# Kernel optimization log

Hardware: AMD Instinct MI355X
Metric: run time of the kernel (lower is better)

## Reference

```python
import jax, jax.numpy as jnp
import numpy as np

S, N_PER, N_FEAT, HID = 4, 12500, 1024, 256
N_STRUCT = 500


def setup_inputs() -> dict:
    key = jax.random.key(0)
    ks = jax.random.split(key, 11)
    sc = 1.0 / np.sqrt(N_FEAT)
    sh = 1.0 / np.sqrt(HID)
    return {
        "features": jax.random.normal(ks[0], (S, N_PER, N_FEAT), jnp.float32),
        "W1": jax.random.normal(ks[1], (S, N_FEAT, HID), jnp.float32) * sc,
        "b1": jax.random.normal(ks[2], (S, HID), jnp.float32) * 0.01,
        "W2": jax.random.normal(ks[3], (S, HID, HID), jnp.float32) * sh,
        "b2": jax.random.normal(ks[4], (S, HID), jnp.float32) * 0.01,
        "W3": jax.random.normal(ks[5], (S, HID, HID), jnp.float32) * sh,
        "b3": jax.random.normal(ks[6], (S, HID), jnp.float32) * 0.01,
        "W4": jax.random.normal(ks[7], (S, HID, 1), jnp.float32) * sh,
        "b4": jax.random.normal(ks[8], (S, 1), jnp.float32) * 0.01,
        "structure_idx": jax.random.randint(ks[9], (S, N_PER), 0, N_STRUCT, jnp.int64 if jax.config.jax_enable_x64 else jnp.int32).astype(jnp.int32),
        "n_structures": N_STRUCT,
    }


def reference(features, W1, b1, W2, b2, W3, b3, W4, b4, structure_idx, n_structures):
    # Per-species 4-layer SiLU MLP applied to species-grouped feature blocks.
    h = jax.nn.silu(jnp.einsum("snf,sfh->snh", features, W1) + b1[:, None, :])
    h = jax.nn.silu(jnp.einsum("snh,shk->snk", h, W2) + b2[:, None, :])
    h = jax.nn.silu(jnp.einsum("snh,shk->snk", h, W3) + b3[:, None, :])
    e = jnp.einsum("snh,sho->sno", h, W4) + b4[:, None, :]  # [S, N_per, 1]
    atomic_energies = e[..., 0].reshape(-1)                  # concat over species
    # index_add_ into per-structure energies
    energies = jax.ops.segment_sum(atomic_energies, structure_idx.reshape(-1), num_segments=n_structures)
    return energies
```

## Files before the change

kernel.cpp:

```cpp
#include <hip/hip_runtime.h>

typedef _Float16 f16;
typedef __attribute__((ext_vector_type(8))) _Float16 f16x8;
typedef __attribute__((ext_vector_type(4))) float f32x4;
typedef unsigned int u32;

#define S_      4
#define NPER    12500
#define NF      1024
#define HID     256
#define NSTRUCT 500
#define TM      64

#define GLB __attribute__((address_space(1)))
#define AS3 __attribute__((address_space(3)))

#define WAIT_VM(N)  asm volatile("s_waitcnt vmcnt(" #N ")" ::: "memory")
#define WAIT_LGKM() asm volatile("s_waitcnt lgkmcnt(0)" ::: "memory")
#define SCHED0()    __builtin_amdgcn_sched_barrier(0)
#define BARRIER()   do { __builtin_amdgcn_s_barrier(); SCHED0(); } while (0)

__global__ __launch_bounds__(256) void transpose_all_kernel(
    const float* __restrict__ W1, const float* __restrict__ W2,
    const float* __restrict__ W3,
    f16* __restrict__ w1t, f16* __restrict__ w2t, f16* __restrict__ w3t)
{
  const int z = blockIdx.z;
  const int layer = z >> 2, sp = z & 3;
  const float* in; f16* out; int K;
  if (layer == 0)      { in = W1; out = w1t; K = NF;  }
  else if (layer == 1) { in = W2; out = w2t; K = HID; }
  else                 { in = W3; out = w3t; K = HID; }
  if (blockIdx.x * 64 >= K) return;

  __shared__ float tile[64][65];
  const float* inp = in + (size_t)sp * K * HID;
  f16* outp = out + (size_t)sp * K * HID;
  const int k0 = blockIdx.x * 64;
  const int n0 = blockIdx.y * 64;
  const int t = threadIdx.x;
  {
    const int lk = t >> 2;
    const int nq = (t & 3) * 16;
    const float* src = inp + (size_t)(k0 + lk) * HID + n0 + nq;
    #pragma unroll
    for (int i = 0; i < 4; ++i) {
      float4 v = *(const float4*)(src + i * 4);
      tile[lk][nq + i * 4 + 0] = v.x;
      tile[lk][nq + i * 4 + 1] = v.y;
      tile[lk][nq + i * 4 + 2] = v.z;
      tile[lk][nq + i * 4 + 3] = v.w;
    }
  }
  __syncthreads();
  {
    const int ln = t >> 2;
    const int kq = (t & 3) * 16;
    f16* dst = outp + (size_t)(n0 + ln) * K + k0 + kq;
    f16x8 a, b;
    #pragma unroll
    for (int j = 0; j < 8; ++j) a[j] = (f16)tile[kq + j][ln];
    #pragma unroll
    for (int j = 0; j < 8; ++j) b[j] = (f16)tile[kq + 8 + j][ln];
    *(f16x8*)dst = a;
    *(f16x8*)(dst + 8) = b;
  }
}


__device__ __forceinline__ void zero_acc(f32x4 (&acc)[4][4]) {
  #pragma unroll
  for (int a = 0; a < 4; ++a)
    #pragma unroll
    for (int b = 0; b < 4; ++b)
      #pragma unroll
      for (int j = 0; j < 4; ++j) acc[a][b][j] = 0.f;
}

__device__ __forceinline__ void stage_w64(char* bS, const char* wbase, int c,
                                          int w, int lane)
{
  #pragma unroll
  for (int i = 0; i < 8; ++i) {
    const int seg  = w * 8 + i;
    const int rloc = lane >> 3;
    const int p    = lane & 7;
    const int row  = seg * 8 + rloc;
    const int slog = p ^ rloc;
    const char* gp = wbase + (size_t)row * (NF * 2) + (size_t)c * 128 + slog * 16;
    char* lp = bS + seg * 1024;
    __builtin_amdgcn_global_load_lds((const GLB u32*)gp, (AS3 u32*)lp, 16, 0, 0);
  }
}

__device__ __forceinline__ void stage_w32(char* wS, const char* wbase, int c,
                                          int w, int lane)
{
  #pragma unroll
  for (int i = 0; i < 4; ++i) {
    const int seg = w * 4 + i;
    const int row = seg * 16 + (lane >> 2);
    const int kbp = lane & 3;
    const int kb  = kbp ^ ((row >> 1) & 3);
    const char* gp = wbase + (size_t)row * (HID * 2) + c * 64 + kb * 16;
    char* lp = wS + seg * 1024;
    __builtin_amdgcn_global_load_lds((const GLB u32*)gp, (AS3 u32*)lp, 16, 0, 0);
  }
}

__device__ __forceinline__ void load_pa(float4 (&pa)[4], const float* fsrcT, int c)
{
  #pragma unroll
  for (int j = 0; j < 4; ++j)
    pa[j] = *(const float4*)(fsrcT + c * 64 + j * 4);
}

__device__ __forceinline__ void stage_feat64(char* aS, const float4 (&pa)[4], int t)
{
  const int r = t >> 2;
  #pragma unroll
  for (int wr = 0; wr < 2; ++wr) {
    f16x8 hv;
    const float4 lo = pa[wr * 2 + 0], hi = pa[wr * 2 + 1];
    hv[0]=(f16)lo.x; hv[1]=(f16)lo.y; hv[2]=(f16)lo.z; hv[3]=(f16)lo.w;
    hv[4]=(f16)hi.x; hv[5]=(f16)hi.y; hv[6]=(f16)hi.z; hv[7]=(f16)hi.w;
    const int slog = (t & 3) * 2 + wr;
    const int p = slog ^ (r & 7);
    *(f16x8*)(aS + r * 128 + p * 16) = hv;
  }
}

__device__ __forceinline__ void mfma64_a(f32x4 (&acc)[4][4], const char* aS,
                                         const char* bS, int w, int g, int l15)
{
  #pragma unroll
  for (int ks = 0; ks < 2; ++ks) {
    f16x8 af[4], bf[4];
    #pragma unroll
    for (int at = 0; at < 4; ++at) {
      const int rr = at * 16 + l15;
      const int p  = (ks * 4 + g) ^ (rr & 7);
      af[at] = *(const f16x8*)(aS + rr * 128 + p * 16);
    }
    #pragma unroll
    for (int bt = 0; bt < 4; ++bt) {
      const int nn = w * 64 + bt * 16 + l15;
      const int p  = (ks * 4 + g) ^ (nn & 7);
      bf[bt] = *(const f16x8*)(bS + nn * 128 + p * 16);
    }
    #pragma unroll
    for (int at = 0; at < 4; ++at)
      #pragma unroll
      for (int bt = 0; bt < 4; ++bt)
        acc[at][bt] = __builtin_amdgcn_mfma_f32_16x16x32_f16(af[at], bf[bt], acc[at][bt], 0, 0, 0);
  }
}

__device__ __forceinline__ void mfma32_h(f32x4 (&acc)[4][4], const char* hL, int c,
                                         const char* wS, int w, int g, int l15)
{
  f16x8 af[4], bf[4];
  #pragma unroll
  for (int at = 0; at < 4; ++at) {
    const int rr = at * 16 + l15;
    af[at] = *(const f16x8*)(hL + ((rr * 512 + c * 64 + g * 16) ^ ((rr & 7) << 4)));
  }
  #pragma unroll
  for (int bt = 0; bt < 4; ++bt) {
    const int nn = w * 64 + bt * 16 + l15;
    bf[bt] = *(const f16x8*)(wS + nn * 64 + ((g ^ ((nn >> 1) & 3)) * 16));
  }
  #pragma unroll
  for (int at = 0; at < 4; ++at)
    #pragma unroll
    for (int bt = 0; bt < 4; ++bt)
      acc[at][bt] = __builtin_amdgcn_mfma_f32_16x16x32_f16(af[at], bf[bt], acc[at][bt], 0, 0, 0);
}

__device__ __forceinline__ void silu_store(f32x4 (&acc)[4][4],
                                           const float* __restrict__ bias,
                                           char* hL, int w, int lane)
{
  const int g = lane >> 4, l15 = lane & 15;
  #pragma unroll
  for (int bt = 0; bt < 4; ++bt) {
    const int col = w * 64 + bt * 16 + l15;
    const float b = bias[col];
    #pragma unroll
    for (int at = 0; at < 4; ++at) {
      #pragma unroll
      for (int j = 0; j < 4; ++j) {
        const int row = at * 16 + g * 4 + j;
        float x = acc[at][bt][j] + b;
        x = x * __builtin_amdgcn_rcpf(1.f + __expf(-x));
        *(f16*)(hL + (((row * HID + col) * 2) ^ ((row & 7) << 4))) = (f16)x;
      }
    }
  }
}

#define L1_STEP(c, ASc, ASn, BSc, BSn, PAset, VMN, DOG, DOPA)   \
  do {                                                           \
    stage_feat64(ASn, PAset, t);                                 \
    if (DOG)  stage_w64(BSn, w1s, (c) + 1, w, lane);             \
    if (DOPA) load_pa(PAset, fsrcT, (c) + 4);                    \
    WAIT_VM(VMN); SCHED0();                                      \
    mfma64_a(acc, ASc, BSc, w, g, l15);                          \
    WAIT_LGKM(); BARRIER();                                      \
  } while (0)

#define HID_ST(c, WSc, WSstg, wsrc, cs)                          \
  do {                                                           \
    WAIT_VM(8); SCHED0();                                        \
    mfma32_h(acc, hL, c, WSc, w, g, l15);                        \
    WAIT_LGKM(); SCHED0();                                       \
    stage_w32(WSstg, wsrc, cs, w, lane);                         \
  } while (0)

__global__ __launch_bounds__(256, 2) void mlp_fused_kernel(
    const float* __restrict__ feats,
    const float* __restrict__ b1g,
    const float* __restrict__ b2g,
    const float* __restrict__ b3g,
    const float* __restrict__ w4g,
    const float* __restrict__ b4g,
    const int*   __restrict__ sidxg,
    const f16*   __restrict__ w1t,
    const f16*   __restrict__ w2t,
    const f16*   __restrict__ w3t,
    float*       __restrict__ outg)
{
  __shared__ char arena[80 * 1024];
  char* aS0 = arena;
  char* aS1 = arena + 8 * 1024;
  char* bS0 = arena + 16 * 1024;
  char* bS1 = arena + 48 * 1024;
  char* hL  = arena;
  char* wS0 = arena + 32 * 1024;
  char* wS1 = arena + 48 * 1024;
  char* wS2 = arena + 64 * 1024;

  const int s    = blockIdx.y;
  const int row0 = blockIdx.x * TM;
  const int t    = threadIdx.x;
  const int lane = t & 63;
  const int w    = t >> 6;
  const int g    = lane >> 4;
  const int l15  = lane & 15;

  const int gr   = row0 + (t >> 2);
  const bool valid = gr < NPER;
  const int grc  = valid ? gr : (NPER - 1);
  const float* fsrcT = feats + ((size_t)s * NPER + grc) * NF + (t & 3) * 16;
  const char*  w1s   = (const char*)(w1t + (size_t)s * HID * NF);
  const char*  w2s   = (const char*)(w2t + (size_t)s * HID * HID);
  const char*  w3s   = (const char*)(w3t + (size_t)s * HID * HID);

  f32x4 acc[4][4];
  zero_acc(acc);

  float4 pf[4], paA[4], paB[4], paC[4];
  load_pa(pf, fsrcT, 0);
  stage_w64(bS0, w1s, 0, w, lane);
  load_pa(paA, fsrcT, 1);
  load_pa(paB, fsrcT, 2);
  load_pa(paC, fsrcT, 3);
  stage_feat64(aS0, pf, t);
  WAIT_LGKM(); BARRIER();

  L1_STEP(0,  aS0, aS1, bS0, bS1, paA, 20, 1, 1);
  L1_STEP(1,  aS1, aS0, bS1, bS0, paB, 16, 1, 1);
  L1_STEP(2,  aS0, aS1, bS0, bS1, paC, 16, 1, 1);
  L1_STEP(3,  aS1, aS0, bS1, bS0, paA, 16, 1, 1);
  L1_STEP(4,  aS0, aS1, bS0, bS1, paB, 16, 1, 1);
  L1_STEP(5,  aS1, aS0, bS1, bS0, paC, 16, 1, 1);
  L1_STEP(6,  aS0, aS1, bS0, bS1, paA, 16, 1, 1);
  L1_STEP(7,  aS1, aS0, bS1, bS0, paB, 16, 1, 1);
  L1_STEP(8,  aS0, aS1, bS0, bS1, paC, 16, 1, 1);
  L1_STEP(9,  aS1, aS0, bS1, bS0, paA, 16, 1, 1);
  L1_STEP(10, aS0, aS1, bS0, bS1, paB, 16, 1, 1);
  L1_STEP(11, aS1, aS0, bS1, bS0, paC, 16, 1, 1);
  L1_STEP(12, aS0, aS1, bS0, bS1, paA, 12, 1, 0);
  L1_STEP(13, aS1, aS0, bS1, bS0, paB,  8, 1, 0);
  L1_STEP(14, aS0, aS1, bS0, bS1, paC,  8, 1, 0);
  {
    stage_w32(wS0, w2s, 0, w, lane);
    WAIT_VM(4); SCHED0();
    mfma64_a(acc, aS1, bS1, w, g, l15);
    WAIT_LGKM(); BARRIER();
  }

  silu_store(acc, b1g + s * HID, hL, w, lane);
  zero_acc(acc);
  stage_w32(wS1, w2s, 1, w, lane);
  stage_w32(wS2, w2s, 2, w, lane);
  WAIT_LGKM(); BARRIER();

  HID_ST(0, wS0, wS0, w2s, 3);
  HID_ST(1, wS1, wS1, w2s, 4);
  HID_ST(2, wS2, wS2, w2s, 5);
  HID_ST(3, wS0, wS0, w2s, 6);
  HID_ST(4, wS1, wS1, w2s, 7);
  HID_ST(5, wS2, wS2, w3s, 0);
  HID_ST(6, wS0, wS0, w3s, 1);
  HID_ST(7, wS1, wS1, w3s, 2);
  BARRIER();
  silu_store(acc, b2g + s * HID, hL, w, lane);
  zero_acc(acc);
  WAIT_LGKM(); BARRIER();

  HID_ST(0, wS2, wS2, w3s, 3);
  HID_ST(1, wS0, wS0, w3s, 4);
  HID_ST(2, wS1, wS1, w3s, 5);
  HID_ST(3, wS2, wS2, w3s, 6);
  HID_ST(4, wS0, wS0, w3s, 7);
  { WAIT_VM(8); SCHED0(); mfma32_h(acc, hL, 5, wS1, w, g, l15); }
  { WAIT_VM(4); SCHED0(); mfma32_h(acc, hL, 6, wS2, w, g, l15); }
  { WAIT_VM(0); SCHED0(); mfma32_h(acc, hL, 7, wS0, w, g, l15); }
  BARRIER();
  silu_store(acc, b3g + s * HID, hL, w, lane);
  WAIT_LGKM(); BARRIER();

  {
    const int row = t >> 2;
    const int q   = t & 3;
    const float* w4 = w4g + s * HID;
    float sum = 0.f;
    #pragma unroll
    for (int j8 = 0; j8 < 64; j8 += 8) {
      const int k = q * 64 + j8;
      f16x8 hv = *(const f16x8*)(hL + (((row * HID + k) * 2) ^ ((row & 7) << 4)));
      float4 wa = *(const float4*)(w4 + k);
      float4 wb = *(const float4*)(w4 + k + 4);
      sum += (float)hv[0] * wa.x + (float)hv[1] * wa.y + (float)hv[2] * wa.z + (float)hv[3] * wa.w
           + (float)hv[4] * wb.x + (float)hv[5] * wb.y + (float)hv[6] * wb.z + (float)hv[7] * wb.w;
    }
    sum += __shfl_xor(sum, 1);
    sum += __shfl_xor(sum, 2);
    if (q == 0 && valid) {
      atomicAdd(&outg[sidxg[s * NPER + gr]], sum + b4g[s]);
    }
  }
}

extern "C" void kernel_launch(void* const* d_in, const int* in_sizes, int n_in,
                              void* d_out, int out_size, void* d_ws, size_t ws_size,
                              hipStream_t stream)
{
  const float* feats = (const float*)d_in[0];
  const float* W1    = (const float*)d_in[1];
  const float* b1    = (const float*)d_in[2];
  const float* W2    = (const float*)d_in[3];
  const float* b2    = (const float*)d_in[4];
  const float* W3    = (const float*)d_in[5];
  const float* b3    = (const float*)d_in[6];
  const float* W4    = (const float*)d_in[7];
  const float* b4    = (const float*)d_in[8];
  const int*   sidx  = (const int*)d_in[9];
  float* out = (float*)d_out;

  f16* w1t = (f16*)d_ws;
  f16* w2t = w1t + (size_t)S_ * HID * NF;
  f16* w3t = w2t + (size_t)S_ * HID * HID;

  hipMemsetAsync(d_out, 0, NSTRUCT * sizeof(float), stream);
  transpose_all_kernel<<<dim3(16, 4, 12), 256, 0, stream>>>(W1, W2, W3, w1t, w2t, w3t);
  mlp_fused_kernel<<<dim3((NPER + TM - 1) / TM, S_), 256, 0, stream>>>(
      feats, b1, b2, b3, W4, b4, sidx, w1t, w2t, w3t, out);
}
```

Baseline: 108.3 us.

## Single-buffer weight LDS stages to cut shared memory and allow three blocks per CU

Replaces the double-buffered W1 tile and triple-buffered W2/W3 tiles with single LDS buffers, shrinking shared memory from 80KB to 48KB and raising launch bounds to 3 blocks per CU. Each step now runs the MFMA on the current buffer, then overwrites that buffer with the next weight chunk. The intent is more resident blocks to hide latency. The cost is that weight loads no longer overlap the MFMA work inside a block, and the vmcnt waits are tightened to match.

After: 192.7 us. +77.9%, slower.

```diff
diff --git a/kernel.cpp b/kernel.cpp
--- a/kernel.cpp
+++ b/kernel.cpp
@@ -199,25 +199,26 @@
   }
 }
 
-#define L1_STEP(c, ASc, ASn, BSc, BSn, PAset, VMN, DOG, DOPA)   \
+#define L1_STEP(c, ASc, ASn, PAset, VMN, DOG, DOPA)              \
   do {                                                           \
+    WAIT_VM(VMN); SCHED0();                                      \
+    mfma64_a(acc, ASc, bS, w, g, l15);                           \
+    WAIT_LGKM(); SCHED0();                                       \
+    if (DOG)  stage_w64(bS, w1s, (c) + 1, w, lane);              \
     stage_feat64(ASn, PAset, t);                                 \
-    if (DOG)  stage_w64(BSn, w1s, (c) + 1, w, lane);             \
     if (DOPA) load_pa(PAset, fsrcT, (c) + 4);                    \
-    WAIT_VM(VMN); SCHED0();                                      \
-    mfma64_a(acc, ASc, BSc, w, g, l15);                          \
     WAIT_LGKM(); BARRIER();                                      \
   } while (0)
 
-#define HID_ST(c, WSc, WSstg, wsrc, cs)                          \
+#define HID_ST(c, wsrc, cs, DOG)                                 \
   do {                                                           \
-    WAIT_VM(8); SCHED0();                                        \
-    mfma32_h(acc, hL, c, WSc, w, g, l15);                        \
+    WAIT_VM(0); SCHED0();                                        \
+    mfma32_h(acc, hL, c, wS, w, g, l15);                         \
     WAIT_LGKM(); SCHED0();                                       \
-    stage_w32(WSstg, wsrc, cs, w, lane);                         \
+    if (DOG) stage_w32(wS, wsrc, cs, w, lane);                   \
   } while (0)
 
-__global__ __launch_bounds__(256, 2) void mlp_fused_kernel(
+__global__ __launch_bounds__(256, 3) void mlp_fused_kernel(
     const float* __restrict__ feats,
     const float* __restrict__ b1g,
     const float* __restrict__ b2g,
@@ -230,15 +231,12 @@
     const f16*   __restrict__ w3t,
     float*       __restrict__ outg)
 {
-  __shared__ char arena[80 * 1024];
+  __shared__ char arena[48 * 1024];
   char* aS0 = arena;
   char* aS1 = arena + 8 * 1024;
-  char* bS0 = arena + 16 * 1024;
-  char* bS1 = arena + 48 * 1024;
+  char* bS  = arena + 16 * 1024;
   char* hL  = arena;
-  char* wS0 = arena + 32 * 1024;
-  char* wS1 = arena + 48 * 1024;
-  char* wS2 = arena + 64 * 1024;
+  char* wS  = arena + 32 * 1024;
 
   const int s    = blockIdx.y;
   const int row0 = blockIdx.x * TM;
@@ -261,62 +259,60 @@
 
   float4 pf[4], paA[4], paB[4], paC[4];
   load_pa(pf, fsrcT, 0);
-  stage_w64(bS0, w1s, 0, w, lane);
+  stage_w64(bS, w1s, 0, w, lane);
   load_pa(paA, fsrcT, 1);
   load_pa(paB, fsrcT, 2);
   load_pa(paC, fsrcT, 3);
   stage_feat64(aS0, pf, t);
   WAIT_LGKM(); BARRIER();
 
-  L1_STEP(0,  aS0, aS1, bS0, bS1, paA, 20, 1, 1);
-  L1_STEP(1,  aS1, aS0, bS1, bS0, paB, 16, 1, 1);
-  L1_STEP(2,  aS0, aS1, bS0, bS1, paC, 16, 1, 1);
-  L1_STEP(3,  aS1, aS0, bS1, bS0, paA, 16, 1, 1);
-  L1_STEP(4,  aS0, aS1, bS0, bS1, paB, 16, 1, 1);
-  L1_STEP(5,  aS1, aS0, bS1, bS0, paC, 16, 1, 1);
-  L1_STEP(6,  aS0, aS1, bS0, bS1, paA, 16, 1, 1);
-  L1_STEP(7,  aS1, aS0, bS1, bS0, paB, 16, 1, 1);
-  L1_STEP(8,  aS0, aS1, bS0, bS1, paC, 16, 1, 1);
-  L1_STEP(9,  aS1, aS0, bS1, bS0, paA, 16, 1, 1);
-  L1_STEP(10, aS0, aS1, bS0, bS1, paB, 16, 1, 1);
-  L1_STEP(11, aS1, aS0, bS1, bS0, paC, 16, 1, 1);
-  L1_STEP(12, aS0, aS1, bS0, bS1, paA, 12, 1, 0);
-  L1_STEP(13, aS1, aS0, bS1, bS0, paB,  8, 1, 0);
-  L1_STEP(14, aS0, aS1, bS0, bS1, paC,  8, 1, 0);
+  L1_STEP(0,  aS0, aS1, paA, 12, 1, 1);
+  L1_STEP(1,  aS1, aS0, paB,  4, 1, 1);
+  L1_STEP(2,  aS0, aS1, paC,  4, 1, 1);
+  L1_STEP(3,  aS1, aS0, paA,  4, 1, 1);
+  L1_STEP(4,  aS0, aS1, paB,  4, 1, 1);
+  L1_STEP(5,  aS1, aS0, paC,  4, 1, 1);
+  L1_STEP(6,  aS0, aS1, paA,  4, 1, 1);
+  L1_STEP(7,  aS1, aS0, paB,  4, 1, 1);
+  L1_STEP(8,  aS0, aS1, paC,  4, 1, 1);
+  L1_STEP(9,  aS1, aS0, paA,  4, 1, 1);
+  L1_STEP(10, aS0, aS1, paB,  4, 1, 1);
+  L1_STEP(11, aS1, aS0, paC,  4, 1, 1);
+  L1_STEP(12, aS0, aS1, paA,  4, 1, 0);
+  L1_STEP(13, aS1, aS0, paB,  0, 1, 0);
+  L1_STEP(14, aS0, aS1, paC,  0, 1, 0);
   {
-    stage_w32(wS0, w2s, 0, w, lane);
-    WAIT_VM(4); SCHED0();
-    mfma64_a(acc, aS1, bS1, w, g, l15);
+    WAIT_VM(0); SCHED0();
+    mfma64_a(acc, aS1, bS, w, g, l15);
     WAIT_LGKM(); BARRIER();
   }
 
+  stage_w32(wS, w2s, 0, w, lane);
   silu_store(acc, b1g + s * HID, hL, w, lane);
   zero_acc(acc);
-  stage_w32(wS1, w2s, 1, w, lane);
-  stage_w32(wS2, w2s, 2, w, lane);
   WAIT_LGKM(); BARRIER();
 
-  HID_ST(0, wS0, wS0, w2s, 3);
-  HID_ST(1, wS1, wS1, w2s, 4);
-  HID_ST(2, wS2, wS2, w2s, 5);
-  HID_ST(3, wS0, wS0, w2s, 6);
-  HID_ST(4, wS1, wS1, w2s, 7);
-  HID_ST(5, wS2, wS2, w3s, 0);
-  HID_ST(6, wS0, wS0, w3s, 1);
-  HID_ST(7, wS1, wS1, w3s, 2);
+  HID_ST(0, w2s, 1, 1);
+  HID_ST(1, w2s, 2, 1);
+  HID_ST(2, w2s, 3, 1);
+  HID_ST(3, w2s, 4, 1);
+  HID_ST(4, w2s, 5, 1);
+  HID_ST(5, w2s, 6, 1);
+  HID_ST(6, w2s, 7, 1);
+  HID_ST(7, w3s, 0, 1);
   BARRIER();
   silu_store(acc, b2g + s * HID, hL, w, lane);
   zero_acc(acc);
   WAIT_LGKM(); BARRIER();
 
-  HID_ST(0, wS2, wS2, w3s, 3);
-  HID_ST(1, wS0, wS0, w3s, 4);
-  HID_ST(2, wS1, wS1, w3s, 5);
-  HID_ST(3, wS2, wS2, w3s, 6);
-  HID_ST(4, wS0, wS0, w3s, 7);
-  { WAIT_VM(8); SCHED0(); mfma32_h(acc, hL, 5, wS1, w, g, l15); }
-  { WAIT_VM(4); SCHED0(); mfma32_h(acc, hL, 6, wS2, w, g, l15); }
-  { WAIT_VM(0); SCHED0(); mfma32_h(acc, hL, 7, wS0, w, g, l15); }
+  HID_ST(0, w3s, 1, 1);
+  HID_ST(1, w3s, 2, 1);
+  HID_ST(2, w3s, 3, 1);
+  HID_ST(3, w3s, 4, 1);
+  HID_ST(4, w3s, 5, 1);
+  HID_ST(5, w3s, 6, 1);
+  HID_ST(6, w3s, 7, 1);
+  HID_ST(7, w3s, 0, 0);
   BARRIER();
   silu_store(acc, b3g + s * HID, hL, w, lane);
   WAIT_LGKM(); BARRIER();
```

## Double row tile to 128 with 512 threads; stream hidden-layer weights via registers

Applied to the files above, without the earlier changes.

The fused MLP kernel now processes 128 rows per block with 8 waves arranged as 2 row groups by 4 column groups. Each W1 tile staged in LDS is therefore reused across twice as many rows, and the layer-1 pipeline switches to a single A buffer with a reordered stage/compute phase. The W2/W3 LDS staging is removed: each wave loads its B fragments for the hidden layers directly from global memory into double-buffered registers. This cuts W1 traffic per row and LDS round-trips for the hidden layers, at the cost of more register pressure, fewer blocks in the grid, and exposed global-load latency in the hidden layers.

New measurement: 183.1 us. +69.0%, slower.

```diff
diff --git a/kernel.cpp b/kernel.cpp
--- a/kernel.cpp
+++ b/kernel.cpp
@@ -10,7 +10,7 @@
 #define NF      1024
 #define HID     256
 #define NSTRUCT 500
-#define TM      64
+#define TM      128
 
 #define GLB __attribute__((address_space(1)))
 #define AS3 __attribute__((address_space(3)))
@@ -81,29 +81,14 @@
                                           int w, int lane)
 {
   #pragma unroll
-  for (int i = 0; i < 8; ++i) {
-    const int seg  = w * 8 + i;
+  for (int i = 0; i < 4; ++i) {
+    const int seg  = w * 4 + i;
     const int rloc = lane >> 3;
     const int p    = lane & 7;
     const int row  = seg * 8 + rloc;
     const int slog = p ^ rloc;
     const char* gp = wbase + (size_t)row * (NF * 2) + (size_t)c * 128 + slog * 16;
     char* lp = bS + seg * 1024;
-    __builtin_amdgcn_global_load_lds((const GLB u32*)gp, (AS3 u32*)lp, 16, 0, 0);
-  }
-}
-
-__device__ __forceinline__ void stage_w32(char* wS, const char* wbase, int c,
-                                          int w, int lane)
-{
-  #pragma unroll
-  for (int i = 0; i < 4; ++i) {
-    const int seg = w * 4 + i;
-    const int row = seg * 16 + (lane >> 2);
-    const int kbp = lane & 3;
-    const int kb  = kbp ^ ((row >> 1) & 3);
-    const char* gp = wbase + (size_t)row * (HID * 2) + c * 64 + kb * 16;
-    char* lp = wS + seg * 1024;
     __builtin_amdgcn_global_load_lds((const GLB u32*)gp, (AS3 u32*)lp, 16, 0, 0);
   }
 }
@@ -131,20 +116,21 @@
 }
 
 __device__ __forceinline__ void mfma64_a(f32x4 (&acc)[4][4], const char* aS,
-                                         const char* bS, int w, int g, int l15)
+                                         const char* bS, int rgrp, int cg,
+                                         int g, int l15)
 {
   #pragma unroll
   for (int ks = 0; ks < 2; ++ks) {
     f16x8 af[4], bf[4];
     #pragma unroll
     for (int at = 0; at < 4; ++at) {
-      const int rr = at * 16 + l15;
+      const int rr = rgrp * 64 + at * 16 + l15;
       const int p  = (ks * 4 + g) ^ (rr & 7);
       af[at] = *(const f16x8*)(aS + rr * 128 + p * 16);
     }
     #pragma unroll
     for (int bt = 0; bt < 4; ++bt) {
-      const int nn = w * 64 + bt * 16 + l15;
+      const int nn = cg * 64 + bt * 16 + l15;
       const int p  = (ks * 4 + g) ^ (nn & 7);
       bf[bt] = *(const f16x8*)(bS + nn * 128 + p * 16);
     }
@@ -156,19 +142,25 @@
   }
 }
 
+__device__ __forceinline__ void load_bh(f16x8 (&bf)[4], const f16* wsrc, int c,
+                                        int cg, int g, int l15)
+{
+  #pragma unroll
+  for (int bt = 0; bt < 4; ++bt) {
+    const int nn = cg * 64 + bt * 16 + l15;
+    bf[bt] = *(const f16x8*)(wsrc + (size_t)nn * HID + c * 32 + g * 8);
+  }
+}
+
 __device__ __forceinline__ void mfma32_h(f32x4 (&acc)[4][4], const char* hL, int c,
-                                         const char* wS, int w, int g, int l15)
-{
-  f16x8 af[4], bf[4];
+                                         const f16x8 (&bf)[4], int rgrp,
+                                         int g, int l15)
+{
+  f16x8 af[4];
   #pragma unroll
   for (int at = 0; at < 4; ++at) {
-    const int rr = at * 16 + l15;
+    const int rr = rgrp * 64 + at * 16 + l15;
     af[at] = *(const f16x8*)(hL + ((rr * 512 + c * 64 + g * 16) ^ ((rr & 7) << 4)));
-  }
-  #pragma unroll
-  for (int bt = 0; bt < 4; ++bt) {
-    const int nn = w * 64 + bt * 16 + l15;
-    bf[bt] = *(const f16x8*)(wS + nn * 64 + ((g ^ ((nn >> 1) & 3)) * 16));
   }
   #pragma unroll
   for (int at = 0; at < 4; ++at)
@@ -179,18 +171,18 @@
 
 __device__ __forceinline__ void silu_store(f32x4 (&acc)[4][4],
                                            const float* __restrict__ bias,
-                                           char* hL, int w, int lane)
+                                           char* hL, int rgrp, int cg, int lane)
 {
   const int g = lane >> 4, l15 = lane & 15;
   #pragma unroll
   for (int bt = 0; bt < 4; ++bt) {
-    const int col = w * 64 + bt * 16 + l15;
+    const int col = cg * 64 + bt * 16 + l15;
     const float b = bias[col];
     #pragma unroll
     for (int at = 0; at < 4; ++at) {
       #pragma unroll
       for (int j = 0; j < 4; ++j) {
-        const int row = at * 16 + g * 4 + j;
+        const int row = rgrp * 64 + at * 16 + g * 4 + j;
         float x = acc[at][bt][j] + b;
         x = x * __builtin_amdgcn_rcpf(1.f + __expf(-x));
         *(f16*)(hL + (((row * HID + col) * 2) ^ ((row & 7) << 4))) = (f16)x;
@@ -199,25 +191,18 @@
   }
 }
 
-#define L1_STEP(c, ASc, ASn, BSc, BSn, PAset, VMN, DOG, DOPA)   \
+#define L1_PH(c, BSc, PAset, DOPA, DOG, VMN)                     \
   do {                                                           \
-    stage_feat64(ASn, PAset, t);                                 \
-    if (DOG)  stage_w64(BSn, w1s, (c) + 1, w, lane);             \
-    if (DOPA) load_pa(PAset, fsrcT, (c) + 4);                    \
+    mfma64_a(acc, aS, BSc, rgrp, cg, g, l15);                    \
+    WAIT_LGKM(); BARRIER();                                      \
+    stage_feat64(aS, PAset, t);                                  \
+    if (DOPA) load_pa(PAset, fsrcT, (c) + 3);                    \
+    if (DOG)  stage_w64(BSc, w1s, (c) + 2, w, lane);             \
     WAIT_VM(VMN); SCHED0();                                      \
-    mfma64_a(acc, ASc, BSc, w, g, l15);                          \
     WAIT_LGKM(); BARRIER();                                      \
   } while (0)
 
-#define HID_ST(c, WSc, WSstg, wsrc, cs)                          \
-  do {                                                           \
-    WAIT_VM(8); SCHED0();                                        \
-    mfma32_h(acc, hL, c, WSc, w, g, l15);                        \
-    WAIT_LGKM(); SCHED0();                                       \
-    stage_w32(WSstg, wsrc, cs, w, lane);                         \
-  } while (0)
-
-__global__ __launch_bounds__(256, 2) void mlp_fused_kernel(
+__global__ __launch_bounds__(512, 4) void mlp_fused_kernel(
     const float* __restrict__ feats,
     const float* __restrict__ b1g,
     const float* __restrict__ b2g,
@@ -231,20 +216,18 @@
     float*       __restrict__ outg)
 {
   __shared__ char arena[80 * 1024];
-  char* aS0 = arena;
-  char* aS1 = arena + 8 * 1024;
+  char* aS  = arena;
   char* bS0 = arena + 16 * 1024;
   char* bS1 = arena + 48 * 1024;
   char* hL  = arena;
-  char* wS0 = arena + 32 * 1024;
-  char* wS1 = arena + 48 * 1024;
-  char* wS2 = arena + 64 * 1024;
 
   const int s    = blockIdx.y;
   const int row0 = blockIdx.x * TM;
   const int t    = threadIdx.x;
   const int lane = t & 63;
   const int w    = t >> 6;
+  const int rgrp = w >> 2;
+  const int cg   = w & 3;
   const int g    = lane >> 4;
   const int l15  = lane & 15;
 
@@ -253,72 +236,72 @@
   const int grc  = valid ? gr : (NPER - 1);
   const float* fsrcT = feats + ((size_t)s * NPER + grc) * NF + (t & 3) * 16;
   const char*  w1s   = (const char*)(w1t + (size_t)s * HID * NF);
-  const char*  w2s   = (const char*)(w2t + (size_t)s * HID * HID);
-  const char*  w3s   = (const char*)(w3t + (size_t)s * HID * HID);
+  const f16*   w2s   = w2t + (size_t)s * HID * HID;
+  const f16*   w3s   = w3t + (size_t)s * HID * HID;
 
   f32x4 acc[4][4];
+  f16x8 bfA[4], bfB[4];
   zero_acc(acc);
 
-  float4 pf[4], paA[4], paB[4], paC[4];
-  load_pa(pf, fsrcT, 0);
-  stage_w64(bS0, w1s, 0, w, lane);
+  float4 pf[4], paA[4], paB[4];
+  load_pa(pf,  fsrcT, 0);
   load_pa(paA, fsrcT, 1);
   load_pa(paB, fsrcT, 2);
-  load_pa(paC, fsrcT, 3);
-  stage_feat64(aS0, pf, t);
+  stage_w64(bS0, w1s, 0, w, lane);
+  stage_w64(bS1, w1s, 1, w, lane);
+  stage_feat64(aS, pf, t);
+  WAIT_VM(4); SCHED0();
   WAIT_LGKM(); BARRIER();
 
-  L1_STEP(0,  aS0, aS1, bS0, bS1, paA, 20, 1, 1);
-  L1_STEP(1,  aS1, aS0, bS1, bS0, paB, 16, 1, 1);
-  L1_STEP(2,  aS0, aS1, bS0, bS1, paC, 16, 1, 1);
-  L1_STEP(3,  aS1, aS0, bS1, bS0, paA, 16, 1, 1);
-  L1_STEP(4,  aS0, aS1, bS0, bS1, paB, 16, 1, 1);
-  L1_STEP(5,  aS1, aS0, bS1, bS0, paC, 16, 1, 1);
-  L1_STEP(6,  aS0, aS1, bS0, bS1, paA, 16, 1, 1);
-  L1_STEP(7,  aS1, aS0, bS1, bS0, paB, 16, 1, 1);
-  L1_STEP(8,  aS0, aS1, bS0, bS1, paC, 16, 1, 1);
-  L1_STEP(9,  aS1, aS0, bS1, bS0, paA, 16, 1, 1);
-  L1_STEP(10, aS0, aS1, bS0, bS1, paB, 16, 1, 1);
-  L1_STEP(11, aS1, aS0, bS1, bS0, paC, 16, 1, 1);
-  L1_STEP(12, aS0, aS1, bS0, bS1, paA, 12, 1, 0);
-  L1_STEP(13, aS1, aS0, bS1, bS0, paB,  8, 1, 0);
-  L1_STEP(14, aS0, aS1, bS0, bS1, paC,  8, 1, 0);
+  L1_PH(0,  bS0, paA, 1, 1, 8);
+  L1_PH(1,  bS1, paB, 1, 1, 8);
+  L1_PH(2,  bS0, paA, 1, 1, 8);
+  L1_PH(3,  bS1, paB, 1, 1, 8);
+  L1_PH(4,  bS0, paA, 1, 1, 8);
+  L1_PH(5,  bS1, paB, 1, 1, 8);
+  L1_PH(6,  bS0, paA, 1, 1, 8);
+  L1_PH(7,  bS1, paB, 1, 1, 8);
+  L1_PH(8,  bS0, paA, 1, 1, 8);
+  L1_PH(9,  bS1, paB, 1, 1, 8);
+  L1_PH(10, bS0, paA, 1, 1, 8);
+  L1_PH(11, bS1, paB, 1, 1, 8);
+  L1_PH(12, bS0, paA, 1, 1, 8);
+  L1_PH(13, bS1, paB, 0, 1, 4);
+  L1_PH(14, bS0, paA, 0, 0, 0);
   {
-    stage_w32(wS0, w2s, 0, w, lane);
-    WAIT_VM(4); SCHED0();
-    mfma64_a(acc, aS1, bS1, w, g, l15);
+    mfma64_a(acc, aS, bS1, rgrp, cg, g, l15);
+    load_bh(bfA, w2s, 0, cg, g, l15);
+    load_bh(bfB, w2s, 1, cg, g, l15);
     WAIT_LGKM(); BARRIER();
   }
 
-  silu_store(acc, b1g + s * HID, hL, w, lane);
-  zero_acc(acc);
-  stage_w32(wS1, w2s, 1, w, lane);
-  stage_w32(wS2, w2s, 2, w, lane);
-  WAIT_LGKM(); BARRIER();
-
-  HID_ST(0, wS0, wS0, w2s, 3);
-  HID_ST(1, wS1, wS1, w2s, 4);
-  HID_ST(2, wS2, wS2, w2s, 5);
-  HID_ST(3, wS0, wS0, w2s, 6);
-  HID_ST(4, wS1, wS1, w2s, 7);
-  HID_ST(5, wS2, wS2, w3s, 0);
-  HID_ST(6, wS0, wS0, w3s, 1);
-  HID_ST(7, wS1, wS1, w3s, 2);
-  BARRIER();
-  silu_store(acc, b2g + s * HID, hL, w, lane);
+  silu_store(acc, b1g + s * HID, hL, rgrp, cg, lane);
   zero_acc(acc);
   WAIT_LGKM(); BARRIER();
 
-  HID_ST(0, wS2, wS2, w3s, 3);
-  HID_ST(1, wS0, wS0, w3s, 4);
-  HID_ST(2, wS1, wS1, w3s, 5);
-  HID_ST(3, wS2, wS2, w3s, 6);
-  HID_ST(4, wS0, wS0, w3s, 7);
-  { WAIT_VM(8); SCHED0(); mfma32_h(acc, hL, 5, wS1, w, g, l15); }
-  { WAIT_VM(4); SCHED0(); mfma32_h(acc, hL, 6, wS2, w, g, l15); }
-  { WAIT_VM(0); SCHED0(); mfma32_h(acc, hL, 7, wS0, w, g, l15); }
+  mfma32_h(acc, hL, 0, bfA, rgrp, g, l15);  load_bh(bfA, w2s, 2, cg, g, l15);
+  mfma32_h(acc, hL, 1, bfB, rgrp, g, l15);  load_bh(bfB, w2s, 3, cg, g, l15);
+  mfma32_h(acc, hL, 2, bfA, rgrp, g, l15);  load_bh(bfA, w2s, 4, cg, g, l15);
+  mfma32_h(acc, hL, 3, bfB, rgrp, g, l15);  load_bh(bfB, w2s, 5, cg, g, l15);
+  mfma32_h(acc, hL, 4, bfA, rgrp, g, l15);  load_bh(bfA, w2s, 6, cg, g, l15);
+  mfma32_h(acc, hL, 5, bfB, rgrp, g, l15);  load_bh(bfB, w2s, 7, cg, g, l15);
+  mfma32_h(acc, hL, 6, bfA, rgrp, g, l15);  load_bh(bfA, w3s, 0, cg, g, l15);
+  mfma32_h(acc, hL, 7, bfB, rgrp, g, l15);  load_bh(bfB, w3s, 1, cg, g, l15);
   BARRIER();
-  silu_store(acc, b3g + s * HID, hL, w, lane);
+  silu_store(acc, b2g + s * HID, hL, rgrp, cg, lane);
+  zero_acc(acc);
+  WAIT_LGKM(); BARRIER();
+
+  mfma32_h(acc, hL, 0, bfA, rgrp, g, l15);  load_bh(bfA, w3s, 2, cg, g, l15);
+  mfma32_h(acc, hL, 1, bfB, rgrp, g, l15);  load_bh(bfB, w3s, 3, cg, g, l15);
+  mfma32_h(acc, hL, 2, bfA, rgrp, g, l15);  load_bh(bfA, w3s, 4, cg, g, l15);
+  mfma32_h(acc, hL, 3, bfB, rgrp, g, l15);  load_bh(bfB, w3s, 5, cg, g, l15);
+  mfma32_h(acc, hL, 4, bfA, rgrp, g, l15);  load_bh(bfA, w3s, 6, cg, g, l15);
+  mfma32_h(acc, hL, 5, bfB, rgrp, g, l15);  load_bh(bfB, w3s, 7, cg, g, l15);
+  mfma32_h(acc, hL, 6, bfA, rgrp, g, l15);
+  mfma32_h(acc, hL, 7, bfB, rgrp, g, l15);
+  BARRIER();
+  silu_store(acc, b3g + s * HID, hL, rgrp, cg, lane);
   WAIT_LGKM(); BARRIER();
 
   {
@@ -365,6 +348,6 @@
 
   hipMemsetAsync(d_out, 0, NSTRUCT * sizeof(float), stream);
   transpose_all_kernel<<<dim3(16, 4, 12), 256, 0, stream>>>(W1, W2, W3, w1t, w2t, w3t);
-  mlp_fused_kernel<<<dim3((NPER + TM - 1) / TM, S_), 256, 0, stream>>>(
+  mlp_fused_kernel<<<dim3((NPER + TM - 1) / TM, S_), 512, 0, stream>>>(
       feats, b1, b2, b3, W4, b4, sidx, w1t, w2t, w3t, out);
 }
```

## Load hidden-layer weights directly into registers instead of staging through LDS

Applied to the files above, without the earlier changes.

Layers 2 and 3 now read the W2/W3 B-fragments straight from global memory into registers, double-buffered in two sets that are prefetched one step ahead. The LDS staging buffers, the swizzled global_load_lds copies and the explicit vmcnt waits are gone. This removes LDS traffic and most waits from the hidden layers, leaving the compiler to insert the waits on the register loads. In exchange each wave fetches its weight slice separately from global or cache, and register pressure rises under the 2-blocks-per-SM launch bound.

After: 117.3 us. 1.08x slower.

```diff
diff --git a/kernel.cpp b/kernel.cpp
--- a/kernel.cpp
+++ b/kernel.cpp
@@ -93,21 +93,6 @@
   }
 }
 
-__device__ __forceinline__ void stage_w32(char* wS, const char* wbase, int c,
-                                          int w, int lane)
-{
-  #pragma unroll
-  for (int i = 0; i < 4; ++i) {
-    const int seg = w * 4 + i;
-    const int row = seg * 16 + (lane >> 2);
-    const int kbp = lane & 3;
-    const int kb  = kbp ^ ((row >> 1) & 3);
-    const char* gp = wbase + (size_t)row * (HID * 2) + c * 64 + kb * 16;
-    char* lp = wS + seg * 1024;
-    __builtin_amdgcn_global_load_lds((const GLB u32*)gp, (AS3 u32*)lp, 16, 0, 0);
-  }
-}
-
 __device__ __forceinline__ void load_pa(float4 (&pa)[4], const float* fsrcT, int c)
 {
   #pragma unroll
@@ -156,19 +141,24 @@
   }
 }
 
+__device__ __forceinline__ void load_bh(f16x8 (&bf)[4], const f16* wsrc, int c,
+                                        int w, int g, int l15)
+{
+  #pragma unroll
+  for (int bt = 0; bt < 4; ++bt) {
+    const int nn = w * 64 + bt * 16 + l15;
+    bf[bt] = *(const f16x8*)(wsrc + (size_t)nn * HID + c * 32 + g * 8);
+  }
+}
+
 __device__ __forceinline__ void mfma32_h(f32x4 (&acc)[4][4], const char* hL, int c,
-                                         const char* wS, int w, int g, int l15)
-{
-  f16x8 af[4], bf[4];
+                                         const f16x8 (&bf)[4], int g, int l15)
+{
+  f16x8 af[4];
   #pragma unroll
   for (int at = 0; at < 4; ++at) {
     const int rr = at * 16 + l15;
     af[at] = *(const f16x8*)(hL + ((rr * 512 + c * 64 + g * 16) ^ ((rr & 7) << 4)));
-  }
-  #pragma unroll
-  for (int bt = 0; bt < 4; ++bt) {
-    const int nn = w * 64 + bt * 16 + l15;
-    bf[bt] = *(const f16x8*)(wS + nn * 64 + ((g ^ ((nn >> 1) & 3)) * 16));
   }
   #pragma unroll
   for (int at = 0; at < 4; ++at)
@@ -207,14 +197,6 @@
     WAIT_VM(VMN); SCHED0();                                      \
     mfma64_a(acc, ASc, BSc, w, g, l15);                          \
     WAIT_LGKM(); BARRIER();                                      \
-  } while (0)
-
-#define HID_ST(c, WSc, WSstg, wsrc, cs)                          \
-  do {                                                           \
-    WAIT_VM(8); SCHED0();                                        \
-    mfma32_h(acc, hL, c, WSc, w, g, l15);                        \
-    WAIT_LGKM(); SCHED0();                                       \
-    stage_w32(WSstg, wsrc, cs, w, lane);                         \
   } while (0)
 
 __global__ __launch_bounds__(256, 2) void mlp_fused_kernel(
@@ -236,9 +218,6 @@
   char* bS0 = arena + 16 * 1024;
   char* bS1 = arena + 48 * 1024;
   char* hL  = arena;
-  char* wS0 = arena + 32 * 1024;
-  char* wS1 = arena + 48 * 1024;
-  char* wS2 = arena + 64 * 1024;
 
   const int s    = blockIdx.y;
   const int row0 = blockIdx.x * TM;
@@ -253,10 +232,11 @@
   const int grc  = valid ? gr : (NPER - 1);
   const float* fsrcT = feats + ((size_t)s * NPER + grc) * NF + (t & 3) * 16;
   const char*  w1s   = (const char*)(w1t + (size_t)s * HID * NF);
-  const char*  w2s   = (const char*)(w2t + (size_t)s * HID * HID);
-  const char*  w3s   = (const char*)(w3t + (size_t)s * HID * HID);
+  const f16*   w2s   = w2t + (size_t)s * HID * HID;
+  const f16*   w3s   = w3t + (size_t)s * HID * HID;
 
   f32x4 acc[4][4];
+  f16x8 bfA[4], bfB[4];
   zero_acc(acc);
 
   float4 pf[4], paA[4], paB[4], paC[4];
@@ -284,39 +264,38 @@
   L1_STEP(13, aS1, aS0, bS1, bS0, paB,  8, 1, 0);
   L1_STEP(14, aS0, aS1, bS0, bS1, paC,  8, 1, 0);
   {
-    stage_w32(wS0, w2s, 0, w, lane);
-    WAIT_VM(4); SCHED0();
+    load_bh(bfA, w2s, 0, w, g, l15);
+    load_bh(bfB, w2s, 1, w, g, l15);
+    WAIT_VM(8); SCHED0();
     mfma64_a(acc, aS1, bS1, w, g, l15);
     WAIT_LGKM(); BARRIER();
   }
 
   silu_store(acc, b1g + s * HID, hL, w, lane);
   zero_acc(acc);
-  stage_w32(wS1, w2s, 1, w, lane);
-  stage_w32(wS2, w2s, 2, w, lane);
   WAIT_LGKM(); BARRIER();
 
-  HID_ST(0, wS0, wS0, w2s, 3);
-  HID_ST(1, wS1, wS1, w2s, 4);
-  HID_ST(2, wS2, wS2, w2s, 5);
-  HID_ST(3, wS0, wS0, w2s, 6);
-  HID_ST(4, wS1, wS1, w2s, 7);
-  HID_ST(5, wS2, wS2, w3s, 0);
-  HID_ST(6, wS0, wS0, w3s, 1);
-  HID_ST(7, wS1, wS1, w3s, 2);
+  mfma32_h(acc, hL, 0, bfA, g, l15);  load_bh(bfA, w2s, 2, w, g, l15);
+  mfma32_h(acc, hL, 1, bfB, g, l15);  load_bh(bfB, w2s, 3, w, g, l15);
+  mfma32_h(acc, hL, 2, bfA, g, l15);  load_bh(bfA, w2s, 4, w, g, l15);
+  mfma32_h(acc, hL, 3, bfB, g, l15);  load_bh(bfB, w2s, 5, w, g, l15);
+  mfma32_h(acc, hL, 4, bfA, g, l15);  load_bh(bfA, w2s, 6, w, g, l15);
+  mfma32_h(acc, hL, 5, bfB, g, l15);  load_bh(bfB, w2s, 7, w, g, l15);
+  mfma32_h(acc, hL, 6, bfA, g, l15);  load_bh(bfA, w3s, 0, w, g, l15);
+  mfma32_h(acc, hL, 7, bfB, g, l15);  load_bh(bfB, w3s, 1, w, g, l15);
   BARRIER();
   silu_store(acc, b2g + s * HID, hL, w, lane);
   zero_acc(acc);
   WAIT_LGKM(); BARRIER();
 
-  HID_ST(0, wS2, wS2, w3s, 3);
-  HID_ST(1, wS0, wS0, w3s, 4);
-  HID_ST(2, wS1, wS1, w3s, 5);
-  HID_ST(3, wS2, wS2, w3s, 6);
-  HID_ST(4, wS0, wS0, w3s, 7);
-  { WAIT_VM(8); SCHED0(); mfma32_h(acc, hL, 5, wS1, w, g, l15); }
-  { WAIT_VM(4); SCHED0(); mfma32_h(acc, hL, 6, wS2, w, g, l15); }
-  { WAIT_VM(0); SCHED0(); mfma32_h(acc, hL, 7, wS0, w, g, l15); }
+  mfma32_h(acc, hL, 0, bfA, g, l15);  load_bh(bfA, w3s, 2, w, g, l15);
+  mfma32_h(acc, hL, 1, bfB, g, l15);  load_bh(bfB, w3s, 3, w, g, l15);
+  mfma32_h(acc, hL, 2, bfA, g, l15);  load_bh(bfA, w3s, 4, w, g, l15);
+  mfma32_h(acc, hL, 3, bfB, g, l15);  load_bh(bfB, w3s, 5, w, g, l15);
+  mfma32_h(acc, hL, 4, bfA, g, l15);  load_bh(bfA, w3s, 6, w, g, l15);
+  mfma32_h(acc, hL, 5, bfB, g, l15);  load_bh(bfB, w3s, 7, w, g, l15);
+  mfma32_h(acc, hL, 6, bfA, g, l15);
+  mfma32_h(acc, hL, 7, bfB, g, l15);
   BARRIER();
   silu_store(acc, b3g + s * HID, hL, w, lane);
   WAIT_LGKM(); BARRIER();
```
